# Optimization experiments

Measured on AMD Instinct MI355X. Metric: run time of the kernel, lower is better.

## Reference

```python
import jax, jax.numpy as jnp
import numpy as np

N = 100000  # nodes


def setup_inputs() -> dict:
    key = jax.random.key(0)
    k0, k1, k2, k3 = jax.random.split(key, 4)
    IN, H, OUT = 256, 256, 128  # in_channels, 2*out_channels, out_channels
    E = 1600000
    x = jax.random.normal(k0, (N, IN), dtype=jnp.float32)
    edge_index = jax.random.randint(k1, (2, E), 0, N, dtype=jnp.int32)
    W1 = jax.random.normal(k2, (IN, H), dtype=jnp.float32) / np.sqrt(IN)
    b1 = jnp.zeros((H,), dtype=jnp.float32)
    W2 = jax.random.normal(k3, (H, OUT), dtype=jnp.float32) / np.sqrt(H)
    b2 = jnp.zeros((OUT,), dtype=jnp.float32)
    return {"x": x, "edge_index": edge_index, "W1": W1, "b1": b1, "W2": W2, "b2": b2}


def _gcn_layer(x, W, b, src, dst, norm):
    # PyG GCNConv: out[i] = sum_{(j->i)} norm_e * (x @ W)[j] + b, over A + I
    h = x @ W
    msg = h[src] * norm[:, None]          # [E+N, F] gathered edge messages
    out = jax.ops.segment_sum(msg, dst, num_segments=N)
    return out + b


def reference(x, edge_index, W1, b1, W2, b2):
    src, dst = edge_index[0], edge_index[1]
    loop = jnp.arange(N, dtype=src.dtype)
    src = jnp.concatenate([src, loop])    # add self-loops
    dst = jnp.concatenate([dst, loop])
    # symmetric normalization: deg computed on target (col) with unit weights
    deg = jax.ops.segment_sum(jnp.ones_like(dst, dtype=x.dtype), dst, num_segments=N)
    dinv = jnp.where(deg > 0, jax.lax.rsqrt(deg), 0.0)
    norm = dinv[src] * dinv[dst]
    h = jax.nn.relu(_gcn_layer(x, W1, b1, src, dst, norm))
    out = jax.nn.relu(_gcn_layer(h, W2, b2, src, dst, norm))
    return out
```

## Files before the change

kernel.cpp:

```cpp
#include <hip/hip_runtime.h>
#include <hip/hip_fp16.h>


typedef _Float16 f16x8 __attribute__((ext_vector_type(8)));
typedef float f32x4 __attribute__((ext_vector_type(4)));

constexpr int SCAN_CHUNK = 2048;

__global__ __launch_bounds__(256) void count_dst_kernel(const int* __restrict__ dst, int E,
                                                        int* __restrict__ cnt) {
    int e = blockIdx.x * 256 + threadIdx.x;
    if (e < E) atomicAdd(&cnt[dst[e]], 1);
}

__global__ __launch_bounds__(256) void dinv_kernel(const int* __restrict__ cnt,
                                                   float* __restrict__ dinv, int N) {
    int i = blockIdx.x * 256 + threadIdx.x;
    if (i < N) dinv[i] = 1.0f / sqrtf((float)(cnt[i] + 1));
}

__global__ __launch_bounds__(256) void scan_phase1(const int* __restrict__ cnt, int N,
                                                   int* __restrict__ bsum) {
    __shared__ int lds[256];
    int tid = threadIdx.x;
    int base = blockIdx.x * SCAN_CHUNK + tid * 8;
    int s = 0;
#pragma unroll
    for (int j = 0; j < 8; ++j) {
        int idx = base + j;
        if (idx < N) s += cnt[idx];
    }
    lds[tid] = s;
    __syncthreads();
    for (int o = 128; o > 0; o >>= 1) {
        if (tid < o) lds[tid] += lds[tid + o];
        __syncthreads();
    }
    if (tid == 0) bsum[blockIdx.x] = lds[0];
}

__global__ void scan_phase2(int* __restrict__ bsum, int nb, int* __restrict__ rowoff,
                            int N, int E) {
    if (threadIdx.x == 0) {
        int run = 0;
        for (int b = 0; b < nb; ++b) {
            int v = bsum[b];
            bsum[b] = run;
            run += v;
        }
        rowoff[N] = E;
    }
}

__global__ __launch_bounds__(256) void scan_phase3(const int* __restrict__ cnt, int N,
                                                   const int* __restrict__ bsum,
                                                   int* __restrict__ rowoff) {
    __shared__ int lds[256];
    int tid = threadIdx.x;
    int base = blockIdx.x * SCAN_CHUNK + tid * 8;
    int v[8];
    int tsum = 0;
#pragma unroll
    for (int j = 0; j < 8; ++j) {
        int idx = base + j;
        v[j] = (idx < N) ? cnt[idx] : 0;
        tsum += v[j];
    }
    lds[tid] = tsum;
    __syncthreads();
    for (int off = 1; off < 256; off <<= 1) {
        int x = (tid >= off) ? lds[tid - off] : 0;
        __syncthreads();
        lds[tid] += x;
        __syncthreads();
    }
    int run = bsum[blockIdx.x] + lds[tid] - tsum;
#pragma unroll
    for (int j = 0; j < 8; ++j) {
        int idx = base + j;
        if (idx < N) rowoff[idx] = run;
        run += v[j];
    }
}

__global__ __launch_bounds__(256) void fill_csr(const int* __restrict__ src,
                                                const int* __restrict__ dst, int E,
                                                const int* __restrict__ rowoff,
                                                int* __restrict__ cursor,
                                                int* __restrict__ col) {
    int e = blockIdx.x * 256 + threadIdx.x;
    if (e < E) {
        int d = dst[e];
        int pos = atomicAdd(&cursor[d], 1);
        col[rowoff[d] + pos] = src[e];
    }
}

__global__ __launch_bounds__(256) void pack_half(const float* __restrict__ in,
                                                 __half* __restrict__ out, int n8) {
    int i = blockIdx.x * 256 + threadIdx.x;
    if (i < n8) {
        float4 a = ((const float4*)in)[(size_t)i * 2];
        float4 b = ((const float4*)in)[(size_t)i * 2 + 1];
        __half2 h[4];
        h[0] = __floats2half2_rn(a.x, a.y);
        h[1] = __floats2half2_rn(a.z, a.w);
        h[2] = __floats2half2_rn(b.x, b.y);
        h[3] = __floats2half2_rn(b.z, b.w);
        ((uint4*)out)[i] = *(const uint4*)h;
    }
}

__global__ __launch_bounds__(256) void pack_w(const float* __restrict__ W,
                                              __half* __restrict__ Wp, int NC, int total) {
    int t = blockIdx.x * 256 + threadIdx.x;
    if (t >= total) return;
    const int NT = NC / 16;
    int lane = t & 63;
    int rest = t >> 6;
    int nt = rest % NT;
    int ks = rest / NT;
    int n = nt * 16 + (lane & 15);
    int k0 = ks * 32 + (lane >> 4) * 8;
    __half tmp[8];
#pragma unroll
    for (int j = 0; j < 8; ++j) tmp[j] = __float2half_rn(W[(size_t)(k0 + j) * NC + n]);
    ((uint4*)Wp)[t] = *(const uint4*)tmp;
}

__global__ __launch_bounds__(64) void aggregate256_h(const __half* __restrict__ xh,
                                                     const float* __restrict__ dinv,
                                                     const int* __restrict__ rowoff,
                                                     const int* __restrict__ col,
                                                     __half* __restrict__ out) {
    int i = blockIdx.x;
    int lane = threadIdx.x;
    float di = dinv[i];
    const uint2* __restrict__ hv = (const uint2*)xh;
    uint2 raw = hv[(size_t)i * 64 + lane];
    float2 f0 = __half22float2(*(const __half2*)&raw.x);
    float2 f1 = __half22float2(*(const __half2*)&raw.y);
    float ax = di * f0.x, ay = di * f0.y, az = di * f1.x, aw = di * f1.y;
    int e0 = rowoff[i], e1 = rowoff[i + 1];
    int e = e0;
    for (; e + 8 <= e1; e += 8) {
        int s[8];
#pragma unroll
        for (int j = 0; j < 8; ++j) s[j] = col[e + j];
        float w[8];
#pragma unroll
        for (int j = 0; j < 8; ++j) w[j] = dinv[s[j]];
        uint2 u[8];
#pragma unroll
        for (int j = 0; j < 8; ++j) u[j] = hv[(size_t)s[j] * 64 + lane];
#pragma unroll
        for (int j = 0; j < 8; ++j) {
            float2 g0 = __half22float2(*(const __half2*)&u[j].x);
            float2 g1 = __half22float2(*(const __half2*)&u[j].y);
            ax = fmaf(w[j], g0.x, ax);
            ay = fmaf(w[j], g0.y, ay);
            az = fmaf(w[j], g1.x, az);
            aw = fmaf(w[j], g1.y, aw);
        }
    }
    for (; e < e1; ++e) {
        int s = col[e];
        float w = dinv[s];
        uint2 u = hv[(size_t)s * 64 + lane];
        float2 g0 = __half22float2(*(const __half2*)&u.x);
        float2 g1 = __half22float2(*(const __half2*)&u.y);
        ax = fmaf(w, g0.x, ax);
        ay = fmaf(w, g0.y, ay);
        az = fmaf(w, g1.x, az);
        aw = fmaf(w, g1.y, aw);
    }
    __half2 h0 = __floats2half2_rn(ax * di, ay * di);
    __half2 h1 = __floats2half2_rn(az * di, aw * di);
    uint2 o;
    o.x = *(const unsigned int*)&h0;
    o.y = *(const unsigned int*)&h1;
    ((uint2*)out)[(size_t)i * 64 + lane] = o;
}

__global__ __launch_bounds__(64) void aggregate128_h_bias_relu(const __half* __restrict__ h,
                                                               const float* __restrict__ dinv,
                                                               const int* __restrict__ rowoff,
                                                               const int* __restrict__ col,
                                                               const float* __restrict__ bias,
                                                               float* __restrict__ out) {
    int i = blockIdx.x;
    int lane = threadIdx.x;
    float di = dinv[i];
    const unsigned int* __restrict__ hv = (const unsigned int*)h;
    float2 v = __half22float2(*(const __half2*)&hv[(size_t)i * 64 + lane]);
    float ax = v.x, ay = v.y;
    int e0 = rowoff[i], e1 = rowoff[i + 1];
    int e = e0;
    for (; e + 8 <= e1; e += 8) {
        int s[8];
#pragma unroll
        for (int j = 0; j < 8; ++j) s[j] = col[e + j];
        unsigned int u[8];
#pragma unroll
        for (int j = 0; j < 8; ++j) u[j] = hv[(size_t)s[j] * 64 + lane];
#pragma unroll
        for (int j = 0; j < 8; ++j) {
            float2 g = __half22float2(*(const __half2*)&u[j]);
            ax += g.x;
            ay += g.y;
        }
    }
    for (; e < e1; ++e) {
        float2 g = __half22float2(*(const __half2*)&hv[(size_t)col[e] * 64 + lane]);
        ax += g.x;
        ay += g.y;
    }
    float2 bb = ((const float2*)bias)[lane];
    float2 r;
    r.x = fmaxf(fmaf(ax, di, bb.x), 0.f);
    r.y = fmaxf(fmaf(ay, di, bb.y), 0.f);
    ((float2*)out)[(size_t)i * 64 + lane] = r;
}

template <int NC, bool BIAS_RELU, bool ROWSCALE>
__global__ __launch_bounds__(256) void gemm_mfma(const __half* __restrict__ A,
                                                 const __half* __restrict__ Wp,
                                                 const float* __restrict__ bias,
                                                 const float* __restrict__ rowscale,
                                                 __half* __restrict__ out, int M) {
    constexpr int NT = NC / 16;
    const int lane = threadIdx.x & 63;
    const int wave = threadIdx.x >> 6;
    const int kg = lane >> 4;
    const int row = blockIdx.x * 64 + wave * 16 + (lane & 15);
    const int rowc = (row < M) ? row : (M - 1);

    f32x4 acc[NT];
#pragma unroll
    for (int nt = 0; nt < NT; ++nt) acc[nt] = {0.f, 0.f, 0.f, 0.f};

    const f16x8* __restrict__ Ap = (const f16x8*)(A + (size_t)rowc * 256 + kg * 8);
    const f16x8* __restrict__ Wf = (const f16x8*)Wp;

#pragma unroll
    for (int ks = 0; ks < 8; ++ks) {
        f16x8 xfrag = Ap[ks * 4];
        const f16x8* wrow = Wf + (size_t)(ks * NT) * 64 + lane;
#pragma unroll
        for (int nt = 0; nt < NT; ++nt) {
            f16x8 wfrag = wrow[nt * 64];
            acc[nt] = __builtin_amdgcn_mfma_f32_16x16x32_f16(wfrag, xfrag, acc[nt], 0, 0, 0);
        }
    }

    if (row < M) {
        float rs = 1.0f;
        if constexpr (ROWSCALE) rs = rowscale[row];
#pragma unroll
        for (int nt = 0; nt < NT; ++nt) {
            const int n0 = nt * 16 + kg * 4;
            f32x4 v = acc[nt];
            if constexpr (BIAS_RELU) {
                float4 bb = *(const float4*)(bias + n0);
                v[0] = fmaxf(v[0] + bb.x, 0.f);
                v[1] = fmaxf(v[1] + bb.y, 0.f);
                v[2] = fmaxf(v[2] + bb.z, 0.f);
                v[3] = fmaxf(v[3] + bb.w, 0.f);
            }
            if constexpr (ROWSCALE) {
                v[0] *= rs; v[1] *= rs; v[2] *= rs; v[3] *= rs;
            }
            __half2 h0 = __floats2half2_rn(v[0], v[1]);
            __half2 h1 = __floats2half2_rn(v[2], v[3]);
            uint2 o;
            o.x = *(const unsigned int*)&h0;
            o.y = *(const unsigned int*)&h1;
            *(uint2*)(out + (size_t)row * NC + n0) = o;
        }
    }
}

extern "C" void kernel_launch(void* const* d_in, const int* in_sizes, int n_in,
                              void* d_out, int out_size, void* d_ws, size_t ws_size,
                              hipStream_t stream) {
    const float* x  = (const float*)d_in[0];
    const int*   ei = (const int*)d_in[1];
    const float* W1 = (const float*)d_in[2];
    const float* b1 = (const float*)d_in[3];
    const float* W2 = (const float*)d_in[4];
    const float* b2 = (const float*)d_in[5];
    float* out = (float*)d_out;

    const int N = in_sizes[0] / 256;
    const int E = in_sizes[1] / 2;
    const int* src = ei;
    const int* dst = ei + E;

    char* ws = (char*)d_ws;
    size_t off = 0;
    auto alloc = [&](size_t bytes) -> char* {
        char* p = ws + off;
        off += (bytes + 255) & ~(size_t)255;
        return p;
    };
    int*    cnt    = (int*)alloc((size_t)N * 4);
    int*    cursor = (int*)alloc((size_t)N * 4);
    int*    rowoff = (int*)alloc((size_t)(N + 1) * 4);
    int*    bsum   = (int*)alloc(4096);
    float*  dinv   = (float*)alloc((size_t)N * 4);
    int*    col    = (int*)alloc((size_t)E * 4);
    __half* Wp1    = (__half*)alloc((size_t)256 * 256 * 2);
    __half* Wp2    = (__half*)alloc((size_t)256 * 128 * 2);
    __half* bufA   = (__half*)alloc((size_t)N * 256 * 2);
    __half* bufB   = (__half*)alloc((size_t)N * 256 * 2);
    __half* xh    = bufA;
    __half* h1h   = bufA;
    __half* buf1h = bufB;
    __half* buf2h = bufB;

    const int NB = (N + SCAN_CHUNK - 1) / SCAN_CHUNK;

    hipMemsetAsync(cnt, 0, (size_t)N * 4, stream);
    hipMemsetAsync(cursor, 0, (size_t)N * 4, stream);

    count_dst_kernel<<<(E + 255) / 256, 256, 0, stream>>>(dst, E, cnt);
    dinv_kernel<<<(N + 255) / 256, 256, 0, stream>>>(cnt, dinv, N);
    scan_phase1<<<NB, 256, 0, stream>>>(cnt, N, bsum);
    scan_phase2<<<1, 64, 0, stream>>>(bsum, NB, rowoff, N, E);
    scan_phase3<<<NB, 256, 0, stream>>>(cnt, N, bsum, rowoff);
    fill_csr<<<(E + 255) / 256, 256, 0, stream>>>(src, dst, E, rowoff, cursor, col);

    pack_w<<<(8 * 16 * 64 + 255) / 256, 256, 0, stream>>>(W1, Wp1, 256, 8 * 16 * 64);
    pack_w<<<(8 * 8 * 64 + 255) / 256, 256, 0, stream>>>(W2, Wp2, 128, 8 * 8 * 64);
    const int n8 = (N * 256) / 8;
    pack_half<<<(n8 + 255) / 256, 256, 0, stream>>>(x, xh, n8);

    aggregate256_h<<<N, 64, 0, stream>>>(xh, dinv, rowoff, col, buf1h);
    const int GB = (N + 63) / 64;
    gemm_mfma<256, true, false><<<GB, 256, 0, stream>>>(buf1h, Wp1, b1, nullptr, h1h, N);

    gemm_mfma<128, false, true><<<GB, 256, 0, stream>>>(h1h, Wp2, nullptr, dinv, buf2h, N);
    aggregate128_h_bias_relu<<<N, 64, 0, stream>>>(buf2h, dinv, rowoff, col, b2, out);
}
```

Measured before the change: 485.6 us.

## Fuse layer-1 aggregation into GEMM and merge prep kernels

Layer-1 aggregation now runs inside the GEMM kernel. Each wave gathers 16 rows into LDS and feeds them straight to MFMA, so the intermediate N x 256 half buffer is never written to or read back from global memory. Counting, x packing and weight packing are merged into one launch, and dinv is computed inside the scan's first phase, which removes several launches. The trade-off is that each wave now walks 16 rows serially with 64 threads per block-wave instead of one row per block, which lowers parallelism and latency hiding for the gather.

```diff
diff --git a/kernel.cpp b/kernel.cpp
--- a/kernel.cpp
+++ b/kernel.cpp
@@ -7,20 +7,61 @@
 
 constexpr int SCAN_CHUNK = 2048;
 
-__global__ __launch_bounds__(256) void count_dst_kernel(const int* __restrict__ dst, int E,
-                                                        int* __restrict__ cnt) {
-    int e = blockIdx.x * 256 + threadIdx.x;
-    if (e < E) atomicAdd(&cnt[dst[e]], 1);
-}
-
-__global__ __launch_bounds__(256) void dinv_kernel(const int* __restrict__ cnt,
-                                                   float* __restrict__ dinv, int N) {
-    int i = blockIdx.x * 256 + threadIdx.x;
-    if (i < N) dinv[i] = 1.0f / sqrtf((float)(cnt[i] + 1));
-}
+
+__device__ inline void pack_w_body(const float* __restrict__ W, __half* __restrict__ Wp,
+                                   int NC, int t) {
+    const int NT = NC / 16;
+    int lane = t & 63;
+    int rest = t >> 6;
+    int nt = rest % NT;
+    int ks = rest / NT;
+    int n = nt * 16 + (lane & 15);
+    int k0 = ks * 32 + (lane >> 4) * 8;
+    __half tmp[8];
+#pragma unroll
+    for (int j = 0; j < 8; ++j) tmp[j] = __float2half_rn(W[(size_t)(k0 + j) * NC + n]);
+    ((uint4*)Wp)[t] = *(const uint4*)tmp;
+}
+
+__global__ __launch_bounds__(256) void prep_kernel(const int* __restrict__ dst, int E,
+                                                   int* __restrict__ cnt,
+                                                   const float* __restrict__ x,
+                                                   __half* __restrict__ xh, int n8,
+                                                   const float* __restrict__ W1,
+                                                   __half* __restrict__ Wp1,
+                                                   const float* __restrict__ W2,
+                                                   __half* __restrict__ Wp2,
+                                                   int nbCount, int nbPack) {
+    const int b = blockIdx.x;
+    const int tid = threadIdx.x;
+    if (b < nbCount) {
+        int e = b * 256 + tid;
+        if (e < E) atomicAdd(&cnt[dst[e]], 1);
+    } else if (b < nbCount + nbPack) {
+        int i = (b - nbCount) * 256 + tid;
+        if (i < n8) {
+            float4 a = ((const float4*)x)[(size_t)i * 2];
+            float4 bb = ((const float4*)x)[(size_t)i * 2 + 1];
+            __half2 h[4];
+            h[0] = __floats2half2_rn(a.x, a.y);
+            h[1] = __floats2half2_rn(a.z, a.w);
+            h[2] = __floats2half2_rn(bb.x, bb.y);
+            h[3] = __floats2half2_rn(bb.z, bb.w);
+            ((uint4*)xh)[i] = *(const uint4*)h;
+        }
+    } else if (b < nbCount + nbPack + 32) {
+        int t = (b - nbCount - nbPack) * 256 + tid;
+        pack_w_body(W1, Wp1, 256, t);
+    } else {
+        int t = (b - nbCount - nbPack - 32) * 256 + tid;
+        pack_w_body(W2, Wp2, 128, t);
+    }
+}
+
 
 __global__ __launch_bounds__(256) void scan_phase1(const int* __restrict__ cnt, int N,
-                                                   int* __restrict__ bsum) {
+                                                   int* __restrict__ bsum,
+                                                   float* __restrict__ dinv) {
     __shared__ int lds[256];
     int tid = threadIdx.x;
     int base = blockIdx.x * SCAN_CHUNK + tid * 8;
@@ -28,7 +69,11 @@
 #pragma unroll
     for (int j = 0; j < 8; ++j) {
         int idx = base + j;
-        if (idx < N) s += cnt[idx];
+        if (idx < N) {
+            int v = cnt[idx];
+            s += v;
+            dinv[idx] = 1.0f / sqrtf((float)(v + 1));
+        }
     }
     lds[tid] = s;
     __syncthreads();
@@ -96,90 +141,154 @@
     }
 }
 
-__global__ __launch_bounds__(256) void pack_half(const float* __restrict__ in,
-                                                 __half* __restrict__ out, int n8) {
-    int i = blockIdx.x * 256 + threadIdx.x;
-    if (i < n8) {
-        float4 a = ((const float4*)in)[(size_t)i * 2];
-        float4 b = ((const float4*)in)[(size_t)i * 2 + 1];
-        __half2 h[4];
-        h[0] = __floats2half2_rn(a.x, a.y);
-        h[1] = __floats2half2_rn(a.z, a.w);
-        h[2] = __floats2half2_rn(b.x, b.y);
-        h[3] = __floats2half2_rn(b.z, b.w);
-        ((uint4*)out)[i] = *(const uint4*)h;
-    }
-}
-
-__global__ __launch_bounds__(256) void pack_w(const float* __restrict__ W,
-                                              __half* __restrict__ Wp, int NC, int total) {
-    int t = blockIdx.x * 256 + threadIdx.x;
-    if (t >= total) return;
-    const int NT = NC / 16;
-    int lane = t & 63;
-    int rest = t >> 6;
-    int nt = rest % NT;
-    int ks = rest / NT;
-    int n = nt * 16 + (lane & 15);
-    int k0 = ks * 32 + (lane >> 4) * 8;
-    __half tmp[8];
-#pragma unroll
-    for (int j = 0; j < 8; ++j) tmp[j] = __float2half_rn(W[(size_t)(k0 + j) * NC + n]);
-    ((uint4*)Wp)[t] = *(const uint4*)tmp;
-}
-
-__global__ __launch_bounds__(64) void aggregate256_h(const __half* __restrict__ xh,
-                                                     const float* __restrict__ dinv,
-                                                     const int* __restrict__ rowoff,
-                                                     const int* __restrict__ col,
-                                                     __half* __restrict__ out) {
-    int i = blockIdx.x;
-    int lane = threadIdx.x;
-    float di = dinv[i];
+__global__ __launch_bounds__(256) void agg_gemm1(const __half* __restrict__ xh,
+                                                 const float* __restrict__ dinv,
+                                                 const int* __restrict__ rowoff,
+                                                 const int* __restrict__ col,
+                                                 const __half* __restrict__ Wp,
+                                                 const float* __restrict__ bias,
+                                                 __half* __restrict__ out, int M) {
+    constexpr int NT = 16;
+    constexpr int PITCH = 264;
+    __shared__ _Float16 hs[4][16][PITCH];
+
+    const int lane = threadIdx.x & 63;
+    const int wave = threadIdx.x >> 6;
+    const int row0 = blockIdx.x * 64 + wave * 16;
     const uint2* __restrict__ hv = (const uint2*)xh;
-    uint2 raw = hv[(size_t)i * 64 + lane];
-    float2 f0 = __half22float2(*(const __half2*)&raw.x);
-    float2 f1 = __half22float2(*(const __half2*)&raw.y);
-    float ax = di * f0.x, ay = di * f0.y, az = di * f1.x, aw = di * f1.y;
-    int e0 = rowoff[i], e1 = rowoff[i + 1];
-    int e = e0;
-    for (; e + 8 <= e1; e += 8) {
-        int s[8];
-#pragma unroll
-        for (int j = 0; j < 8; ++j) s[j] = col[e + j];
-        float w[8];
-#pragma unroll
-        for (int j = 0; j < 8; ++j) w[j] = dinv[s[j]];
-        uint2 u[8];
-#pragma unroll
-        for (int j = 0; j < 8; ++j) u[j] = hv[(size_t)s[j] * 64 + lane];
-#pragma unroll
-        for (int j = 0; j < 8; ++j) {
-            float2 g0 = __half22float2(*(const __half2*)&u[j].x);
-            float2 g1 = __half22float2(*(const __half2*)&u[j].y);
-            ax = fmaf(w[j], g0.x, ax);
-            ay = fmaf(w[j], g0.y, ay);
-            az = fmaf(w[j], g1.x, az);
-            aw = fmaf(w[j], g1.y, aw);
-        }
-    }
-    for (; e < e1; ++e) {
-        int s = col[e];
-        float w = dinv[s];
-        uint2 u = hv[(size_t)s * 64 + lane];
-        float2 g0 = __half22float2(*(const __half2*)&u.x);
-        float2 g1 = __half22float2(*(const __half2*)&u.y);
-        ax = fmaf(w, g0.x, ax);
-        ay = fmaf(w, g0.y, ay);
-        az = fmaf(w, g1.x, az);
-        aw = fmaf(w, g1.y, aw);
-    }
-    __half2 h0 = __floats2half2_rn(ax * di, ay * di);
-    __half2 h1 = __floats2half2_rn(az * di, aw * di);
-    uint2 o;
-    o.x = *(const unsigned int*)&h0;
-    o.y = *(const unsigned int*)&h1;
-    ((uint2*)out)[(size_t)i * 64 + lane] = o;
+
+    for (int r = 0; r < 16; ++r) {
+        int i = row0 + r;
+        if (i >= M) break;
+        float di = dinv[i];
+        uint2 raw = hv[(size_t)i * 64 + lane];
+        float2 f0 = __half22float2(*(const __half2*)&raw.x);
+        float2 f1 = __half22float2(*(const __half2*)&raw.y);
+        float ax = di * f0.x, ay = di * f0.y, az = di * f1.x, aw = di * f1.y;
+        int e0 = rowoff[i], e1 = rowoff[i + 1];
+        int e = e0;
+        for (; e + 8 <= e1; e += 8) {
+            int s[8];
+#pragma unroll
+            for (int j = 0; j < 8; ++j) s[j] = col[e + j];
+            float w[8];
+#pragma unroll
+            for (int j = 0; j < 8; ++j) w[j] = dinv[s[j]];
+            uint2 u[8];
+#pragma unroll
+            for (int j = 0; j < 8; ++j) u[j] = hv[(size_t)s[j] * 64 + lane];
+#pragma unroll
+            for (int j = 0; j < 8; ++j) {
+                float2 g0 = __half22float2(*(const __half2*)&u[j].x);
+                float2 g1 = __half22float2(*(const __half2*)&u[j].y);
+                ax = fmaf(w[j], g0.x, ax);
+                ay = fmaf(w[j], g0.y, ay);
+                az = fmaf(w[j], g1.x, az);
+                aw = fmaf(w[j], g1.y, aw);
+            }
+        }
+        for (; e < e1; ++e) {
+            int s = col[e];
+            float w = dinv[s];
+            uint2 u = hv[(size_t)s * 64 + lane];
+            float2 g0 = __half22float2(*(const __half2*)&u.x);
+            float2 g1 = __half22float2(*(const __half2*)&u.y);
+            ax = fmaf(w, g0.x, ax);
+            ay = fmaf(w, g0.y, ay);
+            az = fmaf(w, g1.x, az);
+            aw = fmaf(w, g1.y, aw);
+        }
+        __half2 h0 = __floats2half2_rn(ax * di, ay * di);
+        __half2 h1 = __floats2half2_rn(az * di, aw * di);
+        uint2 o;
+        o.x = *(const unsigned int*)&h0;
+        o.y = *(const unsigned int*)&h1;
+        *(uint2*)&hs[wave][r][lane * 4] = o;
+    }
+
+    const int kg = lane >> 4;
+    const int rloc = lane & 15;
+    const int row = row0 + rloc;
+
+    f32x4 acc[NT];
+#pragma unroll
+    for (int nt = 0; nt < NT; ++nt) acc[nt] = {0.f, 0.f, 0.f, 0.f};
+
+    const f16x8* __restrict__ Wf = (const f16x8*)Wp;
+#pragma unroll
+    for (int ks = 0; ks < 8; ++ks) {
+        f16x8 xfrag = *(const f16x8*)&hs[wave][rloc][ks * 32 + kg * 8];
+        const f16x8* wrow = Wf + (size_t)(ks * NT) * 64 + lane;
+#pragma unroll
+        for (int nt = 0; nt < NT; ++nt) {
+            f16x8 wfrag = wrow[nt * 64];
+            acc[nt] = __builtin_amdgcn_mfma_f32_16x16x32_f16(wfrag, xfrag, acc[nt], 0, 0, 0);
+        }
+    }
+
+    if (row < M) {
+#pragma unroll
+        for (int nt = 0; nt < NT; ++nt) {
+            const int n0 = nt * 16 + kg * 4;
+            f32x4 v = acc[nt];
+            float4 bb = *(const float4*)(bias + n0);
+            v[0] = fmaxf(v[0] + bb.x, 0.f);
+            v[1] = fmaxf(v[1] + bb.y, 0.f);
+            v[2] = fmaxf(v[2] + bb.z, 0.f);
+            v[3] = fmaxf(v[3] + bb.w, 0.f);
+            __half2 h0 = __floats2half2_rn(v[0], v[1]);
+            __half2 h1 = __floats2half2_rn(v[2], v[3]);
+            uint2 o;
+            o.x = *(const unsigned int*)&h0;
+            o.y = *(const unsigned int*)&h1;
+            *(uint2*)(out + (size_t)row * 256 + n0) = o;
+        }
+    }
+}
+
+__global__ __launch_bounds__(256) void gemm_mfma128(const __half* __restrict__ A,
+                                                    const __half* __restrict__ Wp,
+                                                    const float* __restrict__ rowscale,
+                                                    __half* __restrict__ out, int M) {
+    constexpr int NT = 8;
+    const int lane = threadIdx.x & 63;
+    const int wave = threadIdx.x >> 6;
+    const int kg = lane >> 4;
+    const int row = blockIdx.x * 64 + wave * 16 + (lane & 15);
+    const int rowc = (row < M) ? row : (M - 1);
+
+    f32x4 acc[NT];
+#pragma unroll
+    for (int nt = 0; nt < NT; ++nt) acc[nt] = {0.f, 0.f, 0.f, 0.f};
+
+    const f16x8* __restrict__ Ap = (const f16x8*)(A + (size_t)rowc * 256 + kg * 8);
+    const f16x8* __restrict__ Wf = (const f16x8*)Wp;
+
+#pragma unroll
+    for (int ks = 0; ks < 8; ++ks) {
+        f16x8 xfrag = Ap[ks * 4];
+        const f16x8* wrow = Wf + (size_t)(ks * NT) * 64 + lane;
+#pragma unroll
+        for (int nt = 0; nt < NT; ++nt) {
+            f16x8 wfrag = wrow[nt * 64];
+            acc[nt] = __builtin_amdgcn_mfma_f32_16x16x32_f16(wfrag, xfrag, acc[nt], 0, 0, 0);
+        }
+    }
+
+    if (row < M) {
+        float rs = rowscale[row];
+#pragma unroll
+        for (int nt = 0; nt < NT; ++nt) {
+            const int n0 = nt * 16 + kg * 4;
+            f32x4 v = acc[nt];
+            __half2 h0 = __floats2half2_rn(v[0] * rs, v[1] * rs);
+            __half2 h1 = __floats2half2_rn(v[2] * rs, v[3] * rs);
+            uint2 o;
+            o.x = *(const unsigned int*)&h0;
+            o.y = *(const unsigned int*)&h1;
+            *(uint2*)(out + (size_t)row * 128 + n0) = o;
+        }
+    }
 }
 
 __global__ __launch_bounds__(64) void aggregate128_h_bias_relu(const __half* __restrict__ h,
@@ -220,64 +329,6 @@
     r.x = fmaxf(fmaf(ax, di, bb.x), 0.f);
     r.y = fmaxf(fmaf(ay, di, bb.y), 0.f);
     ((float2*)out)[(size_t)i * 64 + lane] = r;
-}
-
-template <int NC, bool BIAS_RELU, bool ROWSCALE>
-__global__ __launch_bounds__(256) void gemm_mfma(const __half* __restrict__ A,
-                                                 const __half* __restrict__ Wp,
-                                                 const float* __restrict__ bias,
-                                                 const float* __restrict__ rowscale,
-                                                 __half* __restrict__ out, int M) {
-    constexpr int NT = NC / 16;
-    const int lane = threadIdx.x & 63;
-    const int wave = threadIdx.x >> 6;
-    const int kg = lane >> 4;
-    const int row = blockIdx.x * 64 + wave * 16 + (lane & 15);
-    const int rowc = (row < M) ? row : (M - 1);
-
-    f32x4 acc[NT];
-#pragma unroll
-    for (int nt = 0; nt < NT; ++nt) acc[nt] = {0.f, 0.f, 0.f, 0.f};
-
-    const f16x8* __restrict__ Ap = (const f16x8*)(A + (size_t)rowc * 256 + kg * 8);
-    const f16x8* __restrict__ Wf = (const f16x8*)Wp;
-
-#pragma unroll
-    for (int ks = 0; ks < 8; ++ks) {
-        f16x8 xfrag = Ap[ks * 4];
-        const f16x8* wrow = Wf + (size_t)(ks * NT) * 64 + lane;
-#pragma unroll
-        for (int nt = 0; nt < NT; ++nt) {
-            f16x8 wfrag = wrow[nt * 64];
-            acc[nt] = __builtin_amdgcn_mfma_f32_16x16x32_f16(wfrag, xfrag, acc[nt], 0, 0, 0);
-        }
-    }
-
-    if (row < M) {
-        float rs = 1.0f;
-        if constexpr (ROWSCALE) rs = rowscale[row];
-#pragma unroll
-        for (int nt = 0; nt < NT; ++nt) {
-            const int n0 = nt * 16 + kg * 4;
-            f32x4 v = acc[nt];
-            if constexpr (BIAS_RELU) {
-                float4 bb = *(const float4*)(bias + n0);
-                v[0] = fmaxf(v[0] + bb.x, 0.f);
-                v[1] = fmaxf(v[1] + bb.y, 0.f);
-                v[2] = fmaxf(v[2] + bb.z, 0.f);
-                v[3] = fmaxf(v[3] + bb.w, 0.f);
-            }
-            if constexpr (ROWSCALE) {
-                v[0] *= rs; v[1] *= rs; v[2] *= rs; v[3] *= rs;
-            }
-            __half2 h0 = __floats2half2_rn(v[0], v[1]);
-            __half2 h1 = __floats2half2_rn(v[2], v[3]);
-            uint2 o;
-            o.x = *(const unsigned int*)&h0;
-            o.y = *(const unsigned int*)&h1;
-            *(uint2*)(out + (size_t)row * NC + n0) = o;
-        }
-    }
 }
 
 extern "C" void kernel_launch(void* const* d_in, const int* in_sizes, int n_in,
@@ -314,31 +365,29 @@
     __half* bufA   = (__half*)alloc((size_t)N * 256 * 2);
     __half* bufB   = (__half*)alloc((size_t)N * 256 * 2);
     __half* xh    = bufA;
-    __half* h1h   = bufA;
-    __half* buf1h = bufB;
-    __half* buf2h = bufB;
+    __half* buf2h = bufA;
+    __half* h1h   = bufB;
 
     const int NB = (N + SCAN_CHUNK - 1) / SCAN_CHUNK;
+    const int GB = (N + 63) / 64;
 
     hipMemsetAsync(cnt, 0, (size_t)N * 4, stream);
     hipMemsetAsync(cursor, 0, (size_t)N * 4, stream);
 
-    count_dst_kernel<<<(E + 255) / 256, 256, 0, stream>>>(dst, E, cnt);
-    dinv_kernel<<<(N + 255) / 256, 256, 0, stream>>>(cnt, dinv, N);
-    scan_phase1<<<NB, 256, 0, stream>>>(cnt, N, bsum);
+    const int n8 = (N * 256) / 8;
+    const int nbCount = (E + 255) / 256;
+    const int nbPack = (n8 + 255) / 256;
+    const int nbPrep = nbCount + nbPack + 32 + 16;
+    prep_kernel<<<nbPrep, 256, 0, stream>>>(dst, E, cnt, x, xh, n8, W1, Wp1, W2, Wp2,
+                                            nbCount, nbPack);
+
+    scan_phase1<<<NB, 256, 0, stream>>>(cnt, N, bsum, dinv);
     scan_phase2<<<1, 64, 0, stream>>>(bsum, NB, rowoff, N, E);
     scan_phase3<<<NB, 256, 0, stream>>>(cnt, N, bsum, rowoff);
     fill_csr<<<(E + 255) / 256, 256, 0, stream>>>(src, dst, E, rowoff, cursor, col);
 
-    pack_w<<<(8 * 16 * 64 + 255) / 256, 256, 0, stream>>>(W1, Wp1, 256, 8 * 16 * 64);
-    pack_w<<<(8 * 8 * 64 + 255) / 256, 256, 0, stream>>>(W2, Wp2, 128, 8 * 8 * 64);
-    const int n8 = (N * 256) / 8;
-    pack_half<<<(n8 + 255) / 256, 256, 0, stream>>>(x, xh, n8);
-
-    aggregate256_h<<<N, 64, 0, stream>>>(xh, dinv, rowoff, col, buf1h);
-    const int GB = (N + 63) / 64;
-    gemm_mfma<256, true, false><<<GB, 256, 0, stream>>>(buf1h, Wp1, b1, nullptr, h1h, N);
-
-    gemm_mfma<128, false, true><<<GB, 256, 0, stream>>>(h1h, Wp2, nullptr, dinv, buf2h, N);
+    agg_gemm1<<<GB, 256, 0, stream>>>(xh, dinv, rowoff, col, Wp1, b1, h1h, N);
+
+    gemm_mfma128<<<GB, 256, 0, stream>>>(h1h, Wp2, dinv, buf2h, N);
     aggregate128_h_bias_relu<<<N, 64, 0, stream>>>(buf2h, dinv, rowoff, col, b2, out);
 }
```

After: 525.7 us. +8.3%, slower.
